# Performance work log

Hardware: AMD Instinct MI355X
Metric: run time of the kernel (lower is better)

## Reference

```python
import jax, jax.numpy as jnp
import numpy as np

OBS_LEN = 20
N_COORD = 2
HIDDEN = 1024  # z_dim + c_dim = 512 + 512
N = 4096


def setup_inputs() -> dict:
    key = jax.random.key(0)
    ks = jax.random.split(key, 6)
    obs_traj_rel = jax.random.normal(ks[0], (OBS_LEN, N, N_COORD), dtype=jnp.float32)
    pred_lstm_hidden = jax.random.normal(ks[1], (N, HIDDEN), dtype=jnp.float32)
    # LSTMCell params (PyTorch layout): weight_ih [4H, in], weight_hh [4H, H],
    # initialized N(0, 0.1); biases zero (per _initialize_weights).
    W_ih = 0.1 * jax.random.normal(ks[2], (4 * HIDDEN, N_COORD), dtype=jnp.float32)
    W_hh = 0.1 * jax.random.normal(ks[3], (4 * HIDDEN, HIDDEN), dtype=jnp.float32)
    b_ih = jnp.zeros((4 * HIDDEN,), dtype=jnp.float32)
    b_hh = jnp.zeros((4 * HIDDEN,), dtype=jnp.float32)
    # hidden2pos Linear: weight [n_coord, H], bias zero
    W_out = 0.1 * jax.random.normal(ks[4], (N_COORD, HIDDEN), dtype=jnp.float32)
    b_out = jnp.zeros((N_COORD,), dtype=jnp.float32)
    return {
        "obs_traj_rel": obs_traj_rel,
        "pred_lstm_hidden": pred_lstm_hidden,
        "W_ih": W_ih,
        "W_hh": W_hh,
        "b_ih": b_ih,
        "b_hh": b_hh,
        "W_out": W_out,
        "b_out": b_out,
        "variant_feats": 1,
    }


def reference(obs_traj_rel, pred_lstm_hidden, W_ih, W_hh, b_ih, b_hh, W_out, b_out, variant_feats):
    # Step 0 consumes obs[0]; step i>=1 consumes obs[i-1] (per the original loop).
    x_seq = jnp.concatenate([obs_traj_rel[:1], obs_traj_rel[:-1]], axis=0)[..., :N_COORD]
    c0 = jnp.zeros_like(pred_lstm_hidden)

    def step(carry, x_t):
        h, c = carry
        # PyTorch LSTMCell: gates = x W_ih^T + b_ih + h W_hh^T + b_hh, order i,f,g,o
        gates = x_t @ W_ih.T + b_ih + h @ W_hh.T + b_hh
        i, f, g, o = jnp.split(gates, 4, axis=-1)
        c = jax.nn.sigmoid(f) * c + jax.nn.sigmoid(i) * jnp.tanh(g)
        h = jax.nn.sigmoid(o) * jnp.tanh(c)
        out = h @ W_out.T + b_out  # [N, n_coord]
        return (h, c), out

    _, outs = jax.lax.scan(step, (pred_lstm_hidden, c0), x_seq)
    return outs  # [obs_len, N, n_coord]
```

## Files before the change

### kernel.cpp

```cpp
#include <hip/hip_runtime.h>
#include <hip/hip_bf16.h>
#include <stdint.h>

#define N_BATCH 4096
#define HID     1024
#define OBSLEN  20

#define BM  256
#define BHC 64
#define BK  64

using short8 = __attribute__((ext_vector_type(8))) short;
using f32x4  = __attribute__((ext_vector_type(4))) float;

#define AS1 __attribute__((address_space(1)))
#define AS3 __attribute__((address_space(3)))

__device__ __forceinline__ float rcpf(float x) { return __builtin_amdgcn_rcpf(x); }
__device__ __forceinline__ float sigf(float x) { return rcpf(1.f + __expf(-x)); }
__device__ __forceinline__ float tanh_(float x) {
    float a = fminf(15.f, fmaxf(-15.f, x));
    float t = __expf(-2.f * a);
    return (1.f - t) * rcpf(1.f + t);
}
__device__ __forceinline__ unsigned short f2bf(float f) {
    __hip_bfloat16 b = __float2bfloat16(f);
    return *reinterpret_cast<unsigned short*>(&b);
}
__device__ __forceinline__ float bf2f(unsigned short u) {
    unsigned int x = ((unsigned int)u) << 16;
    return __uint_as_float(x);
}

__global__ __launch_bounds__(256) void prep_kernel(
    const float4* __restrict__ Whh, const float4* __restrict__ h0,
    ushort4* __restrict__ Wg, ushort4* __restrict__ hb, float4* __restrict__ c, int n4)
{
    int i = blockIdx.x * 256 + threadIdx.x;
    if (i < n4) {
        float4 w = Whh[i];
        float4 h = h0[i];
        Wg[i] = make_ushort4(f2bf(w.x), f2bf(w.y), f2bf(w.z), f2bf(w.w));
        hb[i] = make_ushort4(f2bf(h.x), f2bf(h.y), f2bf(h.z), f2bf(h.w));
        c[i] = make_float4(0.f, 0.f, 0.f, 0.f);
    }
}

__global__ __launch_bounds__(512, 2) void lstm_step_kernel(
    const ushort* __restrict__ hin,
    const ushort* __restrict__ Wg,
    const float*  __restrict__ xt,
    const float*  __restrict__ Wih,
    const float*  __restrict__ bih,
    const float*  __restrict__ bhh,
    float*        __restrict__ cst,
    ushort*       __restrict__ hout)
{
    __shared__ __align__(16) char lds[131072];
    const int tid  = threadIdx.x;
    const int lane = tid & 63, l15 = lane & 15, l4 = lane >> 4;
    const int wid  = tid >> 6, wr = wid >> 2, wc = wid & 3;
    const int m0   = blockIdx.x * BM;
    const int h0c  = blockIdx.y * BHC;

    const int rowS = tid >> 3;
    const int offS = ((tid & 7) * 16) ^ ((rowS & 7) << 4);
    const ushort* aS = hin + (size_t)(m0 + rowS) * HID + (offS >> 1);
    const ushort* bS = Wg  + (size_t)(h0c + rowS) * HID + (offS >> 1);
    char* aD = lds + tid * 16;
    char* bD = lds + 65536 + tid * 16;

    auto stA = [&](int buf, int kt1, int r) {
        __builtin_amdgcn_global_load_lds(
            (const AS1 void*)(aS + kt1 * BK + (size_t)r * 64 * HID),
            (AS3 void*)(aD + buf * 32768 + r * 8192), 16, 0, 0);
    };
    auto stB = [&](int buf, int kt1, int r) {
        __builtin_amdgcn_global_load_lds(
            (const AS1 void*)(bS + kt1 * BK + (size_t)r * 1024 * HID),
            (AS3 void*)(bD + buf * 32768 + r * 8192), 16, 0, 0);
    };

    const int swz  = (l15 & 7) << 4;
    const int aOff = (wr * 128 + l15) * 128 + ((l4 * 16) ^ swz);
    const int bOff = (wc * 16  + l15) * 128 + ((l4 * 16) ^ swz);

    f32x4 acc[8][4];
#pragma unroll
    for (int f = 0; f < 8; ++f)
#pragma unroll
        for (int g = 0; g < 4; ++g)
            acc[f][g] = (f32x4){0.f, 0.f, 0.f, 0.f};

#pragma unroll
    for (int r = 0; r < 4; ++r) stA(0, 0, r);
#pragma unroll
    for (int r = 0; r < 4; ++r) stB(0, 0, r);

    const int NK = HID / BK;
    for (int kt = 0; kt < NK; ++kt) {
        const int cur = kt & 1, nxt = cur ^ 1;
        const bool st = (kt < NK - 1);
        const char* A = lds + cur * 32768;
        const char* B = lds + 65536 + cur * 32768;

        short8 af[8], bf0, bf1, bf2, bf3;

        asm volatile("s_waitcnt vmcnt(2)" ::: "memory");
        __builtin_amdgcn_s_barrier();
        __builtin_amdgcn_sched_barrier(0);
#pragma unroll
        for (int f = 0; f < 8; ++f)
            af[f] = *(const short8*)(A + aOff + f * 2048);
        bf0 = *(const short8*)(B + bOff);
        bf1 = *(const short8*)(B + bOff + 8192);
        if (st) { stA(nxt, kt + 1, 0); stA(nxt, kt + 1, 1); }
        __builtin_amdgcn_s_setprio(1);
#pragma unroll
        for (int f = 0; f < 8; ++f) {
            acc[f][0] = __builtin_amdgcn_mfma_f32_16x16x32_bf16(af[f], bf0, acc[f][0], 0, 0, 0);
            acc[f][1] = __builtin_amdgcn_mfma_f32_16x16x32_bf16(af[f], bf1, acc[f][1], 0, 0, 0);
        }
        __builtin_amdgcn_s_setprio(0);

        if (st) asm volatile("s_waitcnt vmcnt(2)" ::: "memory");
        else    asm volatile("s_waitcnt vmcnt(0)" ::: "memory");
        __builtin_amdgcn_s_barrier();
        __builtin_amdgcn_sched_barrier(0);
        bf2 = *(const short8*)(B + bOff + 16384);
        bf3 = *(const short8*)(B + bOff + 24576);
        if (st) { stA(nxt, kt + 1, 2); stA(nxt, kt + 1, 3); }
        __builtin_amdgcn_s_setprio(1);
#pragma unroll
        for (int f = 0; f < 8; ++f) {
            acc[f][2] = __builtin_amdgcn_mfma_f32_16x16x32_bf16(af[f], bf2, acc[f][2], 0, 0, 0);
            acc[f][3] = __builtin_amdgcn_mfma_f32_16x16x32_bf16(af[f], bf3, acc[f][3], 0, 0, 0);
        }
        __builtin_amdgcn_s_setprio(0);

#pragma unroll
        for (int f = 0; f < 8; ++f)
            af[f] = *(const short8*)(A + (aOff ^ 64) + f * 2048);
        bf0 = *(const short8*)(B + (bOff ^ 64));
        bf1 = *(const short8*)(B + (bOff ^ 64) + 8192);
        if (st) { stB(nxt, kt + 1, 0); stB(nxt, kt + 1, 1); }
        __builtin_amdgcn_s_setprio(1);
#pragma unroll
        for (int f = 0; f < 8; ++f) {
            acc[f][0] = __builtin_amdgcn_mfma_f32_16x16x32_bf16(af[f], bf0, acc[f][0], 0, 0, 0);
            acc[f][1] = __builtin_amdgcn_mfma_f32_16x16x32_bf16(af[f], bf1, acc[f][1], 0, 0, 0);
        }
        __builtin_amdgcn_s_setprio(0);

        bf2 = *(const short8*)(B + (bOff ^ 64) + 16384);
        bf3 = *(const short8*)(B + (bOff ^ 64) + 24576);
        if (st) { stB(nxt, kt + 1, 2); stB(nxt, kt + 1, 3); }
        __builtin_amdgcn_s_setprio(1);
#pragma unroll
        for (int f = 0; f < 8; ++f) {
            acc[f][2] = __builtin_amdgcn_mfma_f32_16x16x32_bf16(af[f], bf2, acc[f][2], 0, 0, 0);
            acc[f][3] = __builtin_amdgcn_mfma_f32_16x16x32_bf16(af[f], bf3, acc[f][3], 0, 0, 0);
        }
        __builtin_amdgcn_s_setprio(0);
    }

    const int hcg = h0c + wc * 16 + l15;
    float wi0[4], wi1[4], bs_[4];
#pragma unroll
    for (int g = 0; g < 4; ++g) {
        int j = g * HID + hcg;
        wi0[g] = Wih[j * 2 + 0];
        wi1[g] = Wih[j * 2 + 1];
        bs_[g] = bih[j] + bhh[j];
    }
#pragma unroll
    for (int f = 0; f < 8; ++f) {
#pragma unroll
        for (int r = 0; r < 4; ++r) {
            int n = m0 + wr * 128 + f * 16 + l4 * 4 + r;
            float x0 = xt[n * 2 + 0], x1 = xt[n * 2 + 1];
            float gi = acc[f][0][r] + x0 * wi0[0] + x1 * wi1[0] + bs_[0];
            float gf = acc[f][1][r] + x0 * wi0[1] + x1 * wi1[1] + bs_[1];
            float gg = acc[f][2][r] + x0 * wi0[2] + x1 * wi1[2] + bs_[2];
            float go = acc[f][3][r] + x0 * wi0[3] + x1 * wi1[3] + bs_[3];
            float iv = sigf(gi), fv = sigf(gf);
            float gv = tanh_(gg), ov = sigf(go);
            size_t idx = (size_t)n * HID + hcg;
            float cn = fv * cst[idx] + iv * gv;
            cst[idx]  = cn;
            hout[idx] = f2bf(ov * tanh_(cn));
        }
    }
}

__global__ __launch_bounds__(256) void out_proj_kernel(
    const ushort* __restrict__ h, const float* __restrict__ Wout,
    const float* __restrict__ bout, float* __restrict__ outt)
{
    const int wid = threadIdx.x >> 6, lane = threadIdx.x & 63;
    const int row = blockIdx.x * 4 + wid;
    const ushort* hr = h + (size_t)row * HID + lane * 16;
    float a0 = 0.f, a1 = 0.f;
#pragma unroll
    for (int half = 0; half < 2; ++half) {
        short8 hv = *(const short8*)(hr + half * 8);
#pragma unroll
        for (int j = 0; j < 8; ++j) {
            int k = lane * 16 + half * 8 + j;
            float f = bf2f((unsigned short)hv[j]);
            a0 += f * Wout[k];
            a1 += f * Wout[HID + k];
        }
    }
#pragma unroll
    for (int off = 32; off > 0; off >>= 1) {
        a0 += __shfl_down(a0, off);
        a1 += __shfl_down(a1, off);
    }
    if (lane == 0) {
        outt[row * 2 + 0] = a0 + bout[0];
        outt[row * 2 + 1] = a1 + bout[1];
    }
}

extern "C" void kernel_launch(void* const* d_in, const int* in_sizes, int n_in,
                              void* d_out, int out_size, void* d_ws, size_t ws_size,
                              hipStream_t stream) {
    const float* obs  = (const float*)d_in[0];
    const float* h0   = (const float*)d_in[1];
    const float* Wih  = (const float*)d_in[2];
    const float* Whh  = (const float*)d_in[3];
    const float* bih  = (const float*)d_in[4];
    const float* bhh  = (const float*)d_in[5];
    const float* Wout = (const float*)d_in[6];
    const float* bout = (const float*)d_in[7];
    float* out = (float*)d_out;

    char* ws = (char*)d_ws;
    ushort* Wg = (ushort*)(ws);
    ushort* hA = (ushort*)(ws + (8  << 20));
    ushort* hB = (ushort*)(ws + (16 << 20));
    float*  c  = (float* )(ws + (24 << 20));

    prep_kernel<<<4096, 256, 0, stream>>>((const float4*)Whh, (const float4*)h0,
                                          (ushort4*)Wg, (ushort4*)hA, (float4*)c,
                                          N_BATCH * HID / 4);

    ushort* hin = hA;
    ushort* hou = hB;
    for (int t = 0; t < OBSLEN; ++t) {
        const float* xt = obs + (size_t)(t == 0 ? 0 : (t - 1)) * N_BATCH * 2;
        lstm_step_kernel<<<dim3(N_BATCH / BM, HID / BHC), 512, 0, stream>>>(
            hin, Wg, xt, Wih, bih, bhh, c, hou);
        out_proj_kernel<<<N_BATCH / 4, 256, 0, stream>>>(
            hou, Wout, bout, out + (size_t)t * N_BATCH * 2);
        ushort* tmp = hin; hin = hou; hou = tmp;
    }
}
```

Before: 892.4 us.

## Permute W_hh rows into contiguous per-block gate tiles and keep cell state in block-local layout

```diff
diff --git a/kernel.cpp b/kernel.cpp
--- a/kernel.cpp
+++ b/kernel.cpp
@@ -7,7 +7,6 @@
 #define OBSLEN  20
 
 #define BM  256
-#define BHC 64
 #define BK  64
 
 using short8 = __attribute__((ext_vector_type(8))) short;
@@ -38,11 +37,16 @@
 {
     int i = blockIdx.x * 256 + threadIdx.x;
     if (i < n4) {
-        float4 w = Whh[i];
         float4 h = h0[i];
-        Wg[i] = make_ushort4(f2bf(w.x), f2bf(w.y), f2bf(w.z), f2bf(w.w));
         hb[i] = make_ushort4(f2bf(h.x), f2bf(h.y), f2bf(h.z), f2bf(h.w));
         c[i] = make_float4(0.f, 0.f, 0.f, 0.f);
+        int R  = i >> 8, k4 = i & 255;
+        int by = R >> 8, cp = R & 255;
+        int g  = (cp >> 4) & 3;
+        int hl = ((cp >> 6) << 4) | (cp & 15);
+        int orig = g * HID + by * 64 + hl;
+        float4 w = Whh[orig * 256 + k4];
+        Wg[i] = make_ushort4(f2bf(w.x), f2bf(w.y), f2bf(w.z), f2bf(w.w));
     }
 }
 
@@ -61,135 +65,150 @@
     const int lane = tid & 63, l15 = lane & 15, l4 = lane >> 4;
     const int wid  = tid >> 6, wr = wid >> 2, wc = wid & 3;
     const int m0   = blockIdx.x * BM;
-    const int h0c  = blockIdx.y * BHC;
+    const int by   = blockIdx.y;
+    const int bid  = blockIdx.y * (N_BATCH / BM) + blockIdx.x;
 
     const int rowS = tid >> 3;
     const int offS = ((tid & 7) * 16) ^ ((rowS & 7) << 4);
     const ushort* aS = hin + (size_t)(m0 + rowS) * HID + (offS >> 1);
-    const ushort* bS = Wg  + (size_t)(h0c + rowS) * HID + (offS >> 1);
+    const ushort* bS = Wg  + (size_t)(by * 256 + rowS) * HID + (offS >> 1);
     char* aD = lds + tid * 16;
     char* bD = lds + 65536 + tid * 16;
 
-    auto stA = [&](int buf, int kt1, int r) {
+    auto stA = [&](int buf, int k0, int r) {
         __builtin_amdgcn_global_load_lds(
-            (const AS1 void*)(aS + kt1 * BK + (size_t)r * 64 * HID),
+            (const AS1 void*)(aS + k0 + (size_t)r * 64 * HID),
             (AS3 void*)(aD + buf * 32768 + r * 8192), 16, 0, 0);
     };
-    auto stB = [&](int buf, int kt1, int r) {
+    auto stB = [&](int buf, int k0, int r) {
         __builtin_amdgcn_global_load_lds(
-            (const AS1 void*)(bS + kt1 * BK + (size_t)r * 1024 * HID),
+            (const AS1 void*)(bS + k0 + (size_t)r * 64 * HID),
             (AS3 void*)(bD + buf * 32768 + r * 8192), 16, 0, 0);
     };
 
-    const int swz  = (l15 & 7) << 4;
-    const int aOff = (wr * 128 + l15) * 128 + ((l4 * 16) ^ swz);
-    const int bOff = (wc * 16  + l15) * 128 + ((l4 * 16) ^ swz);
+    const int swz   = (l15 & 7) << 4;
+    const int kb0   = (l4 * 16) ^ swz;
+    const int aBase = (wr * 128 + l15) * 128 + kb0;
+    const int bBase = (wc * 64  + l15) * 128 + kb0;
 
     f32x4 acc[8][4];
 #pragma unroll
     for (int f = 0; f < 8; ++f)
 #pragma unroll
-        for (int g = 0; g < 4; ++g)
-            acc[f][g] = (f32x4){0.f, 0.f, 0.f, 0.f};
-
-#pragma unroll
-    for (int r = 0; r < 4; ++r) stA(0, 0, r);
-#pragma unroll
-    for (int r = 0; r < 4; ++r) stB(0, 0, r);
-
+        for (int n = 0; n < 4; ++n)
+            acc[f][n] = (f32x4){0.f, 0.f, 0.f, 0.f};
+
+    stB(0, 0, 0); stB(0, 0, 1); stB(0, 0, 2); stB(0, 0, 3);
+    stA(0, 0, 0); stA(0, 0, 2); stA(0, 0, 1); stA(0, 0, 3);
+
+    short8 af[4], bfr[4];
     const int NK = HID / BK;
     for (int kt = 0; kt < NK; ++kt) {
         const int cur = kt & 1, nxt = cur ^ 1;
         const bool st = (kt < NK - 1);
+        const int k1 = (kt + 1) * BK;
         const char* A = lds + cur * 32768;
         const char* B = lds + 65536 + cur * 32768;
 
-        short8 af[8], bf0, bf1, bf2, bf3;
-
         asm volatile("s_waitcnt vmcnt(2)" ::: "memory");
         __builtin_amdgcn_s_barrier();
         __builtin_amdgcn_sched_barrier(0);
 #pragma unroll
-        for (int f = 0; f < 8; ++f)
-            af[f] = *(const short8*)(A + aOff + f * 2048);
-        bf0 = *(const short8*)(B + bOff);
-        bf1 = *(const short8*)(B + bOff + 8192);
-        if (st) { stA(nxt, kt + 1, 0); stA(nxt, kt + 1, 1); }
-        __builtin_amdgcn_s_setprio(1);
-#pragma unroll
-        for (int f = 0; f < 8; ++f) {
-            acc[f][0] = __builtin_amdgcn_mfma_f32_16x16x32_bf16(af[f], bf0, acc[f][0], 0, 0, 0);
-            acc[f][1] = __builtin_amdgcn_mfma_f32_16x16x32_bf16(af[f], bf1, acc[f][1], 0, 0, 0);
-        }
-        __builtin_amdgcn_s_setprio(0);
-
-        if (st) asm volatile("s_waitcnt vmcnt(2)" ::: "memory");
+        for (int f = 0; f < 4; ++f) af[f]  = *(const short8*)(A + aBase + f * 2048);
+#pragma unroll
+        for (int n = 0; n < 4; ++n) bfr[n] = *(const short8*)(B + bBase + n * 2048);
+        if (st) { stB(nxt, k1, 0); stB(nxt, k1, 1); stB(nxt, k1, 2); }
+        asm volatile("s_waitcnt lgkmcnt(0)" ::: "memory");
+        __builtin_amdgcn_sched_barrier(0);
+        __builtin_amdgcn_s_setprio(1);
+#pragma unroll
+        for (int f = 0; f < 4; ++f)
+#pragma unroll
+            for (int n = 0; n < 4; ++n)
+                acc[f][n] = __builtin_amdgcn_mfma_f32_16x16x32_bf16(af[f], bfr[n], acc[f][n], 0, 0, 0);
+        __builtin_amdgcn_s_setprio(0);
+
+        if (st) asm volatile("s_waitcnt vmcnt(3)" ::: "memory");
         else    asm volatile("s_waitcnt vmcnt(0)" ::: "memory");
         __builtin_amdgcn_s_barrier();
         __builtin_amdgcn_sched_barrier(0);
-        bf2 = *(const short8*)(B + bOff + 16384);
-        bf3 = *(const short8*)(B + bOff + 24576);
-        if (st) { stA(nxt, kt + 1, 2); stA(nxt, kt + 1, 3); }
-        __builtin_amdgcn_s_setprio(1);
-#pragma unroll
-        for (int f = 0; f < 8; ++f) {
-            acc[f][2] = __builtin_amdgcn_mfma_f32_16x16x32_bf16(af[f], bf2, acc[f][2], 0, 0, 0);
-            acc[f][3] = __builtin_amdgcn_mfma_f32_16x16x32_bf16(af[f], bf3, acc[f][3], 0, 0, 0);
-        }
-        __builtin_amdgcn_s_setprio(0);
-
-#pragma unroll
-        for (int f = 0; f < 8; ++f)
-            af[f] = *(const short8*)(A + (aOff ^ 64) + f * 2048);
-        bf0 = *(const short8*)(B + (bOff ^ 64));
-        bf1 = *(const short8*)(B + (bOff ^ 64) + 8192);
-        if (st) { stB(nxt, kt + 1, 0); stB(nxt, kt + 1, 1); }
-        __builtin_amdgcn_s_setprio(1);
-#pragma unroll
-        for (int f = 0; f < 8; ++f) {
-            acc[f][0] = __builtin_amdgcn_mfma_f32_16x16x32_bf16(af[f], bf0, acc[f][0], 0, 0, 0);
-            acc[f][1] = __builtin_amdgcn_mfma_f32_16x16x32_bf16(af[f], bf1, acc[f][1], 0, 0, 0);
-        }
-        __builtin_amdgcn_s_setprio(0);
-
-        bf2 = *(const short8*)(B + (bOff ^ 64) + 16384);
-        bf3 = *(const short8*)(B + (bOff ^ 64) + 24576);
-        if (st) { stB(nxt, kt + 1, 2); stB(nxt, kt + 1, 3); }
-        __builtin_amdgcn_s_setprio(1);
-#pragma unroll
-        for (int f = 0; f < 8; ++f) {
-            acc[f][2] = __builtin_amdgcn_mfma_f32_16x16x32_bf16(af[f], bf2, acc[f][2], 0, 0, 0);
-            acc[f][3] = __builtin_amdgcn_mfma_f32_16x16x32_bf16(af[f], bf3, acc[f][3], 0, 0, 0);
-        }
-        __builtin_amdgcn_s_setprio(0);
-    }
-
-    const int hcg = h0c + wc * 16 + l15;
+#pragma unroll
+        for (int f = 0; f < 4; ++f) af[f] = *(const short8*)(A + aBase + (f + 4) * 2048);
+        if (st) { stB(nxt, k1, 3); stA(nxt, k1, 0); stA(nxt, k1, 2); }
+        asm volatile("s_waitcnt lgkmcnt(0)" ::: "memory");
+        __builtin_amdgcn_sched_barrier(0);
+        __builtin_amdgcn_s_setprio(1);
+#pragma unroll
+        for (int f = 0; f < 4; ++f)
+#pragma unroll
+            for (int n = 0; n < 4; ++n)
+                acc[f + 4][n] = __builtin_amdgcn_mfma_f32_16x16x32_bf16(af[f], bfr[n], acc[f + 4][n], 0, 0, 0);
+        __builtin_amdgcn_s_setprio(0);
+
+        __builtin_amdgcn_s_barrier();
+        __builtin_amdgcn_sched_barrier(0);
+#pragma unroll
+        for (int f = 0; f < 4; ++f) af[f]  = *(const short8*)(A + (aBase ^ 64) + f * 2048);
+#pragma unroll
+        for (int n = 0; n < 4; ++n) bfr[n] = *(const short8*)(B + (bBase ^ 64) + n * 2048);
+        if (st) { stA(nxt, k1, 1); stA(nxt, k1, 3); }
+        asm volatile("s_waitcnt lgkmcnt(0)" ::: "memory");
+        __builtin_amdgcn_sched_barrier(0);
+        __builtin_amdgcn_s_setprio(1);
+#pragma unroll
+        for (int f = 0; f < 4; ++f)
+#pragma unroll
+            for (int n = 0; n < 4; ++n)
+                acc[f][n] = __builtin_amdgcn_mfma_f32_16x16x32_bf16(af[f], bfr[n], acc[f][n], 0, 0, 0);
+        __builtin_amdgcn_s_setprio(0);
+
+        __builtin_amdgcn_s_barrier();
+        __builtin_amdgcn_sched_barrier(0);
+#pragma unroll
+        for (int f = 0; f < 4; ++f) af[f] = *(const short8*)(A + (aBase ^ 64) + (f + 4) * 2048);
+        asm volatile("s_waitcnt lgkmcnt(0)" ::: "memory");
+        __builtin_amdgcn_sched_barrier(0);
+        __builtin_amdgcn_s_setprio(1);
+#pragma unroll
+        for (int f = 0; f < 4; ++f)
+#pragma unroll
+            for (int n = 0; n < 4; ++n)
+                acc[f + 4][n] = __builtin_amdgcn_mfma_f32_16x16x32_bf16(af[f], bfr[n], acc[f + 4][n], 0, 0, 0);
+        __builtin_amdgcn_s_setprio(0);
+    }
+
+    float4* c4 = (float4*)cst + (size_t)bid * 4096;
+    float4 cv[8];
+#pragma unroll
+    for (int f = 0; f < 8; ++f) cv[f] = c4[f * 512 + tid];
+
+    const int hcg = by * 64 + wc * 16 + l15;
     float wi0[4], wi1[4], bs_[4];
 #pragma unroll
-    for (int g = 0; g < 4; ++g) {
-        int j = g * HID + hcg;
-        wi0[g] = Wih[j * 2 + 0];
-        wi1[g] = Wih[j * 2 + 1];
-        bs_[g] = bih[j] + bhh[j];
-    }
+    for (int n = 0; n < 4; ++n) {
+        int j = n * HID + hcg;
+        wi0[n] = Wih[j * 2 + 0];
+        wi1[n] = Wih[j * 2 + 1];
+        bs_[n] = bih[j] + bhh[j];
+    }
+    const float2* xt2 = (const float2*)xt;
 #pragma unroll
     for (int f = 0; f < 8; ++f) {
 #pragma unroll
         for (int r = 0; r < 4; ++r) {
-            int n = m0 + wr * 128 + f * 16 + l4 * 4 + r;
-            float x0 = xt[n * 2 + 0], x1 = xt[n * 2 + 1];
-            float gi = acc[f][0][r] + x0 * wi0[0] + x1 * wi1[0] + bs_[0];
-            float gf = acc[f][1][r] + x0 * wi0[1] + x1 * wi1[1] + bs_[1];
-            float gg = acc[f][2][r] + x0 * wi0[2] + x1 * wi1[2] + bs_[2];
-            float go = acc[f][3][r] + x0 * wi0[3] + x1 * wi1[3] + bs_[3];
+            int nrow = m0 + wr * 128 + f * 16 + l4 * 4 + r;
+            float2 x = xt2[nrow];
+            float gi = acc[f][0][r] + x.x * wi0[0] + x.y * wi1[0] + bs_[0];
+            float gf = acc[f][1][r] + x.x * wi0[1] + x.y * wi1[1] + bs_[1];
+            float gg = acc[f][2][r] + x.x * wi0[2] + x.y * wi1[2] + bs_[2];
+            float go = acc[f][3][r] + x.x * wi0[3] + x.y * wi1[3] + bs_[3];
             float iv = sigf(gi), fv = sigf(gf);
             float gv = tanh_(gg), ov = sigf(go);
-            size_t idx = (size_t)n * HID + hcg;
-            float cn = fv * cst[idx] + iv * gv;
-            cst[idx]  = cn;
-            hout[idx] = f2bf(ov * tanh_(cn));
+            float cn = fv * cv[f][r] + iv * gv;
+            cv[f][r] = cn;
+            hout[(size_t)nrow * HID + hcg] = f2bf(ov * tanh_(cn));
         }
+        c4[f * 512 + tid] = cv[f];
     }
 }
 
@@ -250,7 +269,7 @@
     ushort* hou = hB;
     for (int t = 0; t < OBSLEN; ++t) {
         const float* xt = obs + (size_t)(t == 0 ? 0 : (t - 1)) * N_BATCH * 2;
-        lstm_step_kernel<<<dim3(N_BATCH / BM, HID / BHC), 512, 0, stream>>>(
+        lstm_step_kernel<<<dim3(N_BATCH / BM, (4 * HID) / 256), 512, 0, stream>>>(
             hin, Wg, xt, Wih, bih, bhh, c, hou);
         out_proj_kernel<<<N_BATCH / 4, 256, 0, stream>>>(
             hou, Wout, bout, out + (size_t)t * N_BATCH * 2);
```

Result: faster. 861.0 us (-3.5%).
